# Performance work log

Hardware: AMD Instinct MI355X
Metric: run time of the kernel (lower is better)

The kernel has to match this reference:

```python
import jax, jax.numpy as jnp
import numpy as np

STRIDES = (8, 16, 32)
BINS = 16
NC = 80
ALPHA, GAMMA = 0.25, 2.0
W_CLS, W_IOU, W_DFL = 1.0, 7.5, 1.5
B, MAX_GT = 32, 32
EPS = 1e-7


def setup_inputs() -> dict:
    key = jax.random.key(0)
    k0, k1, k2, k3, k4, k5, k6 = jax.random.split(key, 7)
    p0 = jax.random.normal(k0, (B, 4 * BINS + NC, 80, 80), dtype=jnp.float32)
    p1 = jax.random.normal(k1, (B, 4 * BINS + NC, 40, 40), dtype=jnp.float32)
    p2 = jax.random.normal(k2, (B, 4 * BINS + NC, 20, 20), dtype=jnp.float32)
    # realistic xyxy boxes inside a 640x640 image
    c = jax.random.uniform(k3, (B, MAX_GT, 2), minval=60.0, maxval=580.0)
    wh = jax.random.uniform(k4, (B, MAX_GT, 2), minval=16.0, maxval=120.0)
    gt_bboxes = jnp.concatenate([c - wh / 2, c + wh / 2], axis=-1).astype(jnp.float32)
    gt_labels = jax.random.randint(k5, (B, MAX_GT), 0, NC, dtype=jnp.int32)
    raw = jax.random.randint(k6, (B, 8400), 0, 20 * MAX_GT, dtype=jnp.int32)
    matched_gt_inds = jnp.where(raw < MAX_GT, raw, -1)
    return {"p0": p0, "p1": p1, "p2": p2, "gt_bboxes": gt_bboxes,
            "gt_labels": gt_labels, "matched_gt_inds": matched_gt_inds}


def _decode_scale(p, stride):
    # p: [B, 4*BINS + NC, H, W]
    Bp, C, H, W = p.shape
    dfl = p[:, :4 * BINS].reshape(Bp, 4, BINS, H, W)
    cls = p[:, 4 * BINS:]
    # DFL decode: expectation of softmax over bins, scaled by stride
    prob = jax.nn.softmax(dfl, axis=2)
    proj = jnp.arange(BINS, dtype=p.dtype)
    dist = jnp.einsum('bkchw,c->bkhw', prob, proj) * stride  # [B,4,H,W] in pixels
    ys, xs = jnp.meshgrid(jnp.arange(H), jnp.arange(W), indexing='ij')
    cx = ((xs.astype(p.dtype)) + 0.5) * stride
    cy = ((ys.astype(p.dtype)) + 0.5) * stride
    boxes = jnp.stack([cx - dist[:, 0], cy - dist[:, 1],
                       cx + dist[:, 2], cy + dist[:, 3]], axis=-1).reshape(Bp, H * W, 4)
    cls_logits = cls.transpose(0, 2, 3, 1).reshape(Bp, H * W, NC)
    dfl_flat = dfl.transpose(0, 3, 4, 1, 2).reshape(Bp, H * W, 4, BINS)
    grid = jnp.stack([cx, cy], axis=-1).reshape(H * W, 2)
    smap = jnp.full((H * W,), stride, dtype=p.dtype)
    return cls_logits, dfl_flat, boxes, grid, smap


def reference(p0, p1, p2, gt_bboxes, gt_labels, matched_gt_inds):
    outs = [_decode_scale(p, s) for p, s in zip((p0, p1, p2), STRIDES)]
    scores = jnp.concatenate([o[0] for o in outs], axis=1)   # [B,N,NC]
    dfl = jnp.concatenate([o[1] for o in outs], axis=1)      # [B,N,4,BINS]
    pboxes = jnp.concatenate([o[2] for o in outs], axis=1)   # [B,N,4]
    grid = jnp.concatenate([o[3] for o in outs], axis=0)     # [N,2]
    smap = jnp.concatenate([o[4] for o in outs], axis=0)     # [N]

    pos = matched_gt_inds >= 0                               # [B,N]
    idx = jnp.where(pos, matched_gt_inds, 0)
    lbl = jnp.take_along_axis(gt_labels, idx, axis=1)        # [B,N]
    posf = pos.astype(scores.dtype)
    tgt_scores = jax.nn.one_hot(lbl, NC, dtype=scores.dtype) * posf[..., None]

    # sigmoid focal loss (stable BCE-with-logits)
    prob = jax.nn.sigmoid(scores)
    ce = jnp.maximum(scores, 0) - scores * tgt_scores + jnp.log1p(jnp.exp(-jnp.abs(scores)))
    p_t = prob * tgt_scores + (1 - prob) * (1 - tgt_scores)
    alpha_t = tgt_scores * ALPHA + (1 - tgt_scores) * (1 - ALPHA)
    cls_elem = alpha_t * (1.0 - p_t) ** GAMMA * ce
    num_pos = jnp.maximum(posf.sum(), 1.0)
    loss_cls = cls_elem.sum() / num_pos

    # gather matched GT boxes per anchor
    tboxes = jnp.take_along_axis(gt_bboxes, idx[..., None], axis=1)  # [B,N,4]
    gx, gy = grid[None, :, 0], grid[None, :, 1]
    l = jnp.clip(gx - tboxes[..., 0], 0.0)
    t = jnp.clip(gy - tboxes[..., 1], 0.0)
    r = jnp.clip(tboxes[..., 2] - gx, 0.0)
    b_ = jnp.clip(tboxes[..., 3] - gy, 0.0)
    dists = jnp.stack([l, t, r, b_], axis=-1) / smap[None, :, None]   # [B,N,4]
    tb = jnp.clip(dists, 0.0, BINS - 1 - 1e-6)
    lo = jnp.floor(tb).astype(jnp.int32)
    hi = jnp.minimum(lo + 1, BINS - 1)
    a = tb - lo.astype(tb.dtype)
    # soft two-bin DFL target (vectorized form of the scatter_add loop)
    tdist = (jax.nn.one_hot(lo, BINS, dtype=dfl.dtype) * (1.0 - a)[..., None]
             + jax.nn.one_hot(hi, BINS, dtype=dfl.dtype) * a[..., None])   # [B,N,4,BINS]
    logp = jax.nn.log_softmax(dfl, axis=-1)
    dfl_elem = -(tdist * logp).sum(-1)                                # [B,N,4]
    loss_dfl = (dfl_elem * posf[..., None]).sum() / (num_pos * 4.0)

    # IoU loss on positives
    ix1 = jnp.maximum(pboxes[..., 0], tboxes[..., 0])
    iy1 = jnp.maximum(pboxes[..., 1], tboxes[..., 1])
    ix2 = jnp.minimum(pboxes[..., 2], tboxes[..., 2])
    iy2 = jnp.minimum(pboxes[..., 3], tboxes[..., 3])
    inter = jnp.clip(ix2 - ix1, 0.0) * jnp.clip(iy2 - iy1, 0.0)
    area_p = jnp.clip(pboxes[..., 2] - pboxes[..., 0], 0.0) * jnp.clip(pboxes[..., 3] - pboxes[..., 1], 0.0)
    area_t = jnp.clip(tboxes[..., 2] - tboxes[..., 0], 0.0) * jnp.clip(tboxes[..., 3] - tboxes[..., 1], 0.0)
    iou = inter / (area_p + area_t - inter + EPS)
    loss_iou = ((1.0 - iou) * posf).sum() / num_pos

    total = W_CLS * loss_cls + W_IOU * loss_iou + W_DFL * loss_dfl
    return total
```

## Files before the change

kernel.cpp:

```cpp
#include <hip/hip_runtime.h>
#include <math.h>

#define NCLS 80
#define BINS 16
#define BATCH 32
#define MAX_GT 32
#define NA 8400
#define AN (BATCH * NA)
#define NT 2100
#define NB_DFL 1050
#define NB_CLS 2560
#define NSLOT 64
#define ALPHA_C 0.25f
#define W_CLS 1.0
#define W_IOU 7.5
#define W_DFL 1.5
#define EPS_F 1e-7f


__device__ __forceinline__ void block_reduce_atomic(float val, double* __restrict__ target)
{
    __shared__ float s[4];
    __syncthreads();
    #pragma unroll
    for (int o = 32; o > 0; o >>= 1) val += __shfl_down(val, o);
    const int wave = threadIdx.x >> 6, lane = threadIdx.x & 63;
    if (lane == 0) s[wave] = val;
    __syncthreads();
    if (threadIdx.x == 0) atomicAdd(target, (double)(s[0] + s[1] + s[2] + s[3]));
}

__device__ __forceinline__ float focal_elem(float s, float tt)
{
    float e   = __expf(-fabsf(s));
    float inv = 1.f / (1.f + e);
    float prob = (s >= 0.f) ? inv : e * inv;
    float ce  = fmaxf(s, 0.f) - s * tt + __logf(1.f + e);
    float p_t = prob * tt + (1.f - prob) * (1.f - tt);
    float alpha_t = tt * ALPHA_C + (1.f - tt) * (1.f - ALPHA_C);
    float om = 1.f - p_t;
    return alpha_t * om * om * ce;
}

__global__ __launch_bounds__(256) void yolo_prep(
    const int* __restrict__ matched, const int* __restrict__ gt_labels,
    signed char* __restrict__ lblmap, double* __restrict__ acc)
{
    if (blockIdx.x == 0) acc[threadIdx.x] = 0.0;
    const int qid = blockIdx.x * 256 + threadIdx.x;
    if (qid >= AN / 4) return;
    const int a0 = qid * 4;
    const int b  = a0 / NA;
    const int4 m4 = *(const int4*)(matched + a0);
    const int mm[4] = {m4.x, m4.y, m4.z, m4.w};
    char4 o;
    o.x = (mm[0] >= 0) ? (signed char)gt_labels[b * MAX_GT + mm[0]] : (signed char)-1;
    o.y = (mm[1] >= 0) ? (signed char)gt_labels[b * MAX_GT + mm[1]] : (signed char)-1;
    o.z = (mm[2] >= 0) ? (signed char)gt_labels[b * MAX_GT + mm[2]] : (signed char)-1;
    o.w = (mm[3] >= 0) ? (signed char)gt_labels[b * MAX_GT + mm[3]] : (signed char)-1;
    *(char4*)(lblmap + a0) = o;
}

__global__ __launch_bounds__(256) void yolo_mega(
    const float* __restrict__ p0, const float* __restrict__ p1, const float* __restrict__ p2,
    const float* __restrict__ gt_bboxes, const int* __restrict__ matched,
    const signed char* __restrict__ lblmap, double* __restrict__ acc)
{
    const int bid  = blockIdx.x;
    const int slot = bid & (NSLOT - 1);

    if (bid < NB_DFL) {
        __shared__ float spd[64][4][4];
        const int gdt = bid * 256 + (int)threadIdx.x;
        const int k   = gdt & 3;
        const int qg  = gdt >> 2;
        const int b   = qg / NT;
        const int t   = qg - b * NT;

        const float* p; int HW, off, gbase, h, w0; float stride;
        if (t < 1600)      { p = p0; HW = 6400; off = t * 4;          gbase = 0;    stride = 8.f;
                             h = t / 20;  w0 = (t - h * 20) * 4; }
        else if (t < 2000) { p = p1; HW = 1600; off = (t - 1600) * 4; gbase = 6400; stride = 16.f;
                             int u = t - 1600; h = u / 10; w0 = (u - h * 10) * 4; }
        else               { p = p2; HW = 400;  off = (t - 2000) * 4; gbase = 8000; stride = 32.f;
                             int u = t - 2000; h = u / 5;  w0 = (u - h * 5) * 4; }
        const float inv_s = 1.f / stride;
        const float cy = ((float)h + 0.5f) * stride;

        const float* pc = p + (size_t)(b * 144 + k * BINS) * HW + off;
        float v[BINS][4];
        #pragma unroll
        for (int i = 0; i < BINS; ++i) {
            float4 q = *(const float4*)(pc + (size_t)i * HW);
            v[i][0] = q.x; v[i][1] = q.y; v[i][2] = q.z; v[i][3] = q.w;
        }
        const int4 m4 = *(const int4*)(matched + (size_t)b * NA + gbase + off);
        const int mm[4] = {m4.x, m4.y, m4.z, m4.w};
        bool pos[4]; float4 tbv[4]; float tdv[4];
        #pragma unroll
        for (int j = 0; j < 4; ++j) {
            pos[j] = (mm[j] >= 0);
            int idx = pos[j] ? mm[j] : 0;
            tbv[j] = *(const float4*)(gt_bboxes + ((size_t)b * MAX_GT + idx) * 4);
            float cx = ((float)(w0 + j) + 0.5f) * stride;
            float d = (k == 0) ? (cx - tbv[j].x) : (k == 1) ? (cy - tbv[j].y)
                    : (k == 2) ? (tbv[j].z - cx) : (tbv[j].w - cy);
            tdv[j] = fmaxf(d, 0.f) * inv_s;
        }

        float part = 0.f;
        float pd[4];
        #pragma unroll
        for (int j = 0; j < 4; ++j) {
            float tval = fminf(tdv[j], (float)(BINS - 1) - 1e-6f);
            int   lo = (int)floorf(tval);
            float fr = tval - (float)lo;
            float mx = v[0][j];
            #pragma unroll
            for (int i = 1; i < BINS; ++i) mx = fmaxf(mx, v[i][j]);
            float se = 0.f, we = 0.f, vlo = 0.f, vhi = 0.f;
            #pragma unroll
            for (int i = 0; i < BINS; ++i) {
                float e = __expf(v[i][j] - mx);
                se += e;
                we += (float)i * e;
                vlo = (i == lo)     ? v[i][j] : vlo;
                vhi = (i == lo + 1) ? v[i][j] : vhi;
            }
            pd[j] = (we / se) * stride;
            if (pos[j]) {
                float lse = mx + __logf(se);
                part += -((1.f - fr) * (vlo - lse) + fr * (vhi - lse));
            }
        }
        *(float4*)&spd[threadIdx.x >> 2][k][0] = make_float4(pd[0], pd[1], pd[2], pd[3]);
        __syncthreads();

        float iou_part = 0.f, cnt = 0.f;
        if (k == 0) {
            const int g = threadIdx.x >> 2;
            #pragma unroll
            for (int j = 0; j < 4; ++j) {
                if (pos[j]) {
                    float cx = ((float)(w0 + j) + 0.5f) * stride;
                    float px1 = cx - spd[g][0][j], py1 = cy - spd[g][1][j];
                    float px2 = cx + spd[g][2][j], py2 = cy + spd[g][3][j];
                    float4 tb = tbv[j];
                    float ix1 = fmaxf(px1, tb.x), iy1 = fmaxf(py1, tb.y);
                    float ix2 = fminf(px2, tb.z), iy2 = fminf(py2, tb.w);
                    float inter  = fmaxf(ix2 - ix1, 0.f) * fmaxf(iy2 - iy1, 0.f);
                    float area_p = fmaxf(px2 - px1, 0.f) * fmaxf(py2 - py1, 0.f);
                    float area_t = fmaxf(tb.z - tb.x, 0.f) * fmaxf(tb.w - tb.y, 0.f);
                    float iou = inter / (area_p + area_t - inter + EPS_F);
                    iou_part += 1.f - iou;
                    cnt += 1.f;
                }
            }
        }
        block_reduce_atomic(part,     &acc[2 * NSLOT + slot]);
        block_reduce_atomic(iou_part, &acc[1 * NSLOT + slot]);
        block_reduce_atomic(cnt,      &acc[3 * NSLOT + slot]);
    } else {
        const int cbid = bid - NB_DFL;
        const int b = cbid / NCLS;
        const int c = cbid - b * NCLS;
        const size_t cls_ch = (size_t)(b * 144 + 4 * BINS + c);
        const signed char* lb0 = lblmap + b * NA;

        float4 q[9];
        char4  l4[9];
        const float* pl0 = p0 + cls_ch * 6400;
        #pragma unroll
        for (int i = 0; i < 6; ++i) {
            int off = (i * 256 + (int)threadIdx.x) * 4;
            q[i]  = *(const float4*)(pl0 + off);
            l4[i] = *(const char4*)(lb0 + off);
        }
        #pragma unroll
        for (int i = 6; i < 9; ++i) {
            int t  = i * 256 + (int)threadIdx.x;
            int tc = (t < NT) ? t : 0;
            const float* p; int HW, off, gbase;
            if (tc < 1600)      { p = p0; HW = 6400; off = tc * 4;          gbase = 0;    }
            else if (tc < 2000) { p = p1; HW = 1600; off = (tc - 1600) * 4; gbase = 6400; }
            else                { p = p2; HW = 400;  off = (tc - 2000) * 4; gbase = 8000; }
            q[i]  = *(const float4*)(p + cls_ch * HW + off);
            l4[i] = *(const char4*)(lb0 + gbase + off);
        }

        float part = 0.f;
        #pragma unroll
        for (int i = 0; i < 9; ++i) {
            const bool valid = (i < 8) || (i * 256 + (int)threadIdx.x < NT);
            const float s4[4]  = {q[i].x, q[i].y, q[i].z, q[i].w};
            const int   lbl[4] = {l4[i].x, l4[i].y, l4[i].z, l4[i].w};
            float sum = 0.f;
            #pragma unroll
            for (int j = 0; j < 4; ++j)
                sum += focal_elem(s4[j], (c == lbl[j]) ? 1.f : 0.f);
            part += valid ? sum : 0.f;
        }
        block_reduce_atomic(part, &acc[0 * NSLOT + slot]);
    }
}

__global__ __launch_bounds__(256) void yolo_loss_fused(
    const float* __restrict__ p0, const float* __restrict__ p1, const float* __restrict__ p2,
    const float* __restrict__ gt_bboxes, const int* __restrict__ gt_labels,
    const int* __restrict__ matched, double* __restrict__ acc)
{
    const int a = blockIdx.x * blockDim.x + threadIdx.x;
    const int b = blockIdx.y;
    const int slot = blockIdx.x & (NSLOT - 1);
    float cls_acc = 0.f, iou_acc = 0.f, dfl_acc = 0.f, pos_cnt = 0.f;
    if (a < NA) {
        const float* p; int HW, W; float stride; int off;
        if (a < 6400)      { p = p0; HW = 6400; W = 80; stride = 8.f;  off = a; }
        else if (a < 8000) { p = p1; HW = 1600; W = 40; stride = 16.f; off = a - 6400; }
        else               { p = p2; HW = 400;  W = 20; stride = 32.f; off = a - 8000; }
        const int h = off / W, w = off - h * W;
        const float cx = ((float)w + 0.5f) * stride, cy = ((float)h + 0.5f) * stride;
        const float* pb = p + ((size_t)b * 144) * (size_t)HW + (size_t)off;
        const int m = matched[(size_t)b * NA + a];
        const bool pos = (m >= 0);
        const int idx = pos ? m : 0;
        const int lbl = gt_labels[b * MAX_GT + idx];
        const float* tbp = gt_bboxes + ((size_t)b * MAX_GT + idx) * 4;
        const float tx1 = tbp[0], ty1 = tbp[1], tx2 = tbp[2], ty2 = tbp[3];
        float tdist[4] = {fmaxf(cx - tx1, 0.f) / stride, fmaxf(cy - ty1, 0.f) / stride,
                          fmaxf(tx2 - cx, 0.f) / stride, fmaxf(ty2 - cy, 0.f) / stride};
        float pdv[4]; float dfl_sum = 0.f;
        #pragma unroll
        for (int k = 0; k < 4; ++k) {
            float tv = fminf(tdist[k], (float)(BINS - 1) - 1e-6f);
            int lo = (int)floorf(tv);
            float fr = tv - (float)lo;
            const float* pc = pb + (size_t)(k * BINS) * HW;
            float v[BINS];
            #pragma unroll
            for (int i = 0; i < BINS; ++i) v[i] = pc[(size_t)i * HW];
            float mx = v[0];
            #pragma unroll
            for (int i = 1; i < BINS; ++i) mx = fmaxf(mx, v[i]);
            float se = 0.f, we = 0.f, vlo = 0.f, vhi = 0.f;
            #pragma unroll
            for (int i = 0; i < BINS; ++i) {
                float e = __expf(v[i] - mx);
                se += e; we += (float)i * e;
                vlo = (i == lo) ? v[i] : vlo;
                vhi = (i == lo + 1) ? v[i] : vhi;
            }
            pdv[k] = (we / se) * stride;
            if (pos) { float lse = mx + __logf(se); dfl_sum += -((1.f - fr) * (vlo - lse) + fr * (vhi - lse)); }
        }
        const float* pcls = pb + (size_t)(4 * BINS) * HW;
        #pragma unroll 4
        for (int c = 0; c < NCLS; ++c)
            cls_acc += focal_elem(pcls[(size_t)c * HW], (pos && c == lbl) ? 1.f : 0.f);
        if (pos) {
            float px1 = cx - pdv[0], py1 = cy - pdv[1], px2 = cx + pdv[2], py2 = cy + pdv[3];
            float ix1 = fmaxf(px1, tx1), iy1 = fmaxf(py1, ty1);
            float ix2 = fminf(px2, tx2), iy2 = fminf(py2, ty2);
            float inter  = fmaxf(ix2 - ix1, 0.f) * fmaxf(iy2 - iy1, 0.f);
            float area_p = fmaxf(px2 - px1, 0.f) * fmaxf(py2 - py1, 0.f);
            float area_t = fmaxf(tx2 - tx1, 0.f) * fmaxf(ty2 - ty1, 0.f);
            float iou = inter / (area_p + area_t - inter + EPS_F);
            iou_acc = 1.f - iou; dfl_acc = dfl_sum; pos_cnt = 1.f;
        }
    }
    block_reduce_atomic(cls_acc, &acc[0 * NSLOT + slot]);
    block_reduce_atomic(iou_acc, &acc[1 * NSLOT + slot]);
    block_reduce_atomic(dfl_acc, &acc[2 * NSLOT + slot]);
    block_reduce_atomic(pos_cnt, &acc[3 * NSLOT + slot]);
}

__global__ void yolo_loss_finalize(const double* __restrict__ acc, float* __restrict__ out)
{
    double s[4] = {0.0, 0.0, 0.0, 0.0};
    for (int q = 0; q < 4; ++q)
        for (int i = 0; i < NSLOT; ++i) s[q] += acc[q * NSLOT + i];
    double np = s[3] < 1.0 ? 1.0 : s[3];
    double total = W_CLS * s[0] / np + W_IOU * s[1] / np + W_DFL * s[2] / (np * 4.0);
    out[0] = (float)total;
}

extern "C" void kernel_launch(void* const* d_in, const int* in_sizes, int n_in,
                              void* d_out, int out_size, void* d_ws, size_t ws_size,
                              hipStream_t stream)
{
    const float* p0        = (const float*)d_in[0];
    const float* p1        = (const float*)d_in[1];
    const float* p2        = (const float*)d_in[2];
    const float* gt_bboxes = (const float*)d_in[3];
    const int*   gt_labels = (const int*)d_in[4];
    const int*   matched   = (const int*)d_in[5];
    float*  out = (float*)d_out;

    const size_t accBytes = 4 * NSLOT * sizeof(double);
    double*      acc    = (double*)d_ws;
    signed char* lblmap = (signed char*)((char*)d_ws + accBytes);
    const size_t need = accBytes + (size_t)AN;

    if (ws_size >= need) {
        yolo_prep<<<(AN / 4 + 255) / 256, 256, 0, stream>>>(matched, gt_labels, lblmap, acc);
        yolo_mega<<<NB_DFL + NB_CLS, 256, 0, stream>>>(p0, p1, p2, gt_bboxes, matched,
                                                       lblmap, acc);
    } else {
        (void)hipMemsetAsync(acc, 0, accBytes, stream);
        dim3 g((NA + 255) / 256, BATCH);
        yolo_loss_fused<<<g, 256, 0, stream>>>(p0, p1, p2, gt_bboxes, gt_labels, matched, acc);
    }
    yolo_loss_finalize<<<1, 1, 0, stream>>>(acc, out);
}
```

Measured before the change: 213.5 us.

## Use 1024-thread blocks with online softmax for DFL and split class planes

Blocks of the fused loss kernel grow from 256 to 1024 threads. In the DFL branch, each of the four side groups now covers 256 quads. The 16-bin softmax becomes an online, streaming max/sum instead of holding all 64 values in registers, which cuts register pressure so more waves fit. The class branch splits each plane into two halves handled by a strided loop rather than fully unrolled preloads. Block reductions now sum 16 wave partials. The trade-offs are extra exp work from the online rescaling, lower memory-level parallelism per thread, and a second gt_bboxes load for the IoU step.

```diff
diff --git a/kernel.cpp b/kernel.cpp
--- a/kernel.cpp
+++ b/kernel.cpp
@@ -8,8 +8,9 @@
 #define NA 8400
 #define AN (BATCH * NA)
 #define NT 2100
-#define NB_DFL 1050
-#define NB_CLS 2560
+#define NQG (BATCH * NT)
+#define NB_DFL 263
+#define NB_CLS 5120
 #define NSLOT 64
 #define ALPHA_C 0.25f
 #define W_CLS 1.0
@@ -18,7 +19,24 @@
 #define EPS_F 1e-7f
 
 
-__device__ __forceinline__ void block_reduce_atomic(float val, double* __restrict__ target)
+__device__ __forceinline__ void block_reduce_atomic_16(float val, double* __restrict__ target)
+{
+    __shared__ float s[16];
+    __syncthreads();
+    #pragma unroll
+    for (int o = 32; o > 0; o >>= 1) val += __shfl_down(val, o);
+    const int wave = threadIdx.x >> 6, lane = threadIdx.x & 63;
+    if (lane == 0) s[wave] = val;
+    __syncthreads();
+    if (threadIdx.x == 0) {
+        float t = 0.f;
+        #pragma unroll
+        for (int i = 0; i < 16; ++i) t += s[i];
+        atomicAdd(target, (double)t);
+    }
+}
+
+__device__ __forceinline__ void block_reduce_atomic_4(float val, double* __restrict__ target)
 {
     __shared__ float s[4];
     __syncthreads();
@@ -40,6 +58,17 @@
     float alpha_t = tt * ALPHA_C + (1.f - tt) * (1.f - ALPHA_C);
     float om = 1.f - p_t;
     return alpha_t * om * om * ce;
+}
+
+__device__ __forceinline__ void quad_map(int t, int& HW, int& off, int& gbase,
+                                         int& h, int& w0, float& stride)
+{
+    if (t < 1600)      { HW = 6400; off = t * 4;          gbase = 0;    stride = 8.f;
+                         h = t / 20;  w0 = (t - h * 20) * 4; }
+    else if (t < 2000) { HW = 1600; off = (t - 1600) * 4; gbase = 6400; stride = 16.f;
+                         int u = t - 1600; h = u / 10; w0 = (u - h * 10) * 4; }
+    else               { HW = 400;  off = (t - 2000) * 4; gbase = 8000; stride = 32.f;
+                         int u = t - 2000; h = u / 5;  w0 = (u - h * 5) * 4; }
 }
 
 __global__ __launch_bounds__(256) void yolo_prep(
@@ -61,7 +90,7 @@
     *(char4*)(lblmap + a0) = o;
 }
 
-__global__ __launch_bounds__(256) void yolo_mega(
+__global__ __launch_bounds__(1024, 8) void yolo_mega(
     const float* __restrict__ p0, const float* __restrict__ p1, const float* __restrict__ p2,
     const float* __restrict__ gt_bboxes, const int* __restrict__ matched,
     const signed char* __restrict__ lblmap, double* __restrict__ acc)
@@ -70,82 +99,89 @@
     const int slot = bid & (NSLOT - 1);
 
     if (bid < NB_DFL) {
-        __shared__ float spd[64][4][4];
-        const int gdt = bid * 256 + (int)threadIdx.x;
-        const int k   = gdt & 3;
-        const int qg  = gdt >> 2;
-        const int b   = qg / NT;
-        const int t   = qg - b * NT;
-
-        const float* p; int HW, off, gbase, h, w0; float stride;
-        if (t < 1600)      { p = p0; HW = 6400; off = t * 4;          gbase = 0;    stride = 8.f;
-                             h = t / 20;  w0 = (t - h * 20) * 4; }
-        else if (t < 2000) { p = p1; HW = 1600; off = (t - 1600) * 4; gbase = 6400; stride = 16.f;
-                             int u = t - 1600; h = u / 10; w0 = (u - h * 10) * 4; }
-        else               { p = p2; HW = 400;  off = (t - 2000) * 4; gbase = 8000; stride = 32.f;
-                             int u = t - 2000; h = u / 5;  w0 = (u - h * 5) * 4; }
+        __shared__ float4 spd[4][256];
+        const int local = threadIdx.x & 255;
+        const int k     = threadIdx.x >> 8;
+        const int qg    = bid * 256 + local;
+        const bool valid = (qg < NQG);
+        const int qv = valid ? qg : 0;
+        const int b  = qv / NT;
+        const int t  = qv - b * NT;
+
+        int HW, off, gbase, h, w0; float stride;
+        quad_map(t, HW, off, gbase, h, w0, stride);
         const float inv_s = 1.f / stride;
         const float cy = ((float)h + 0.5f) * stride;
-
-        const float* pc = p + (size_t)(b * 144 + k * BINS) * HW + off;
-        float v[BINS][4];
-        #pragma unroll
-        for (int i = 0; i < BINS; ++i) {
-            float4 q = *(const float4*)(pc + (size_t)i * HW);
-            v[i][0] = q.x; v[i][1] = q.y; v[i][2] = q.z; v[i][3] = q.w;
-        }
+        const float* p = (t < 1600) ? p0 : (t < 2000) ? p1 : p2;
+
         const int4 m4 = *(const int4*)(matched + (size_t)b * NA + gbase + off);
         const int mm[4] = {m4.x, m4.y, m4.z, m4.w};
-        bool pos[4]; float4 tbv[4]; float tdv[4];
+        int lo[4]; float fr[4]; bool pos[4];
         #pragma unroll
         for (int j = 0; j < 4; ++j) {
             pos[j] = (mm[j] >= 0);
             int idx = pos[j] ? mm[j] : 0;
-            tbv[j] = *(const float4*)(gt_bboxes + ((size_t)b * MAX_GT + idx) * 4);
+            float4 tb = *(const float4*)(gt_bboxes + ((size_t)b * MAX_GT + idx) * 4);
             float cx = ((float)(w0 + j) + 0.5f) * stride;
-            float d = (k == 0) ? (cx - tbv[j].x) : (k == 1) ? (cy - tbv[j].y)
-                    : (k == 2) ? (tbv[j].z - cx) : (tbv[j].w - cy);
-            tdv[j] = fmaxf(d, 0.f) * inv_s;
+            float d = (k == 0) ? (cx - tb.x) : (k == 1) ? (cy - tb.y)
+                    : (k == 2) ? (tb.z - cx) : (tb.w - cy);
+            float tval = fminf(fmaxf(d, 0.f) * inv_s, (float)(BINS - 1) - 1e-6f);
+            lo[j] = (int)floorf(tval);
+            fr[j] = tval - (float)lo[j];
+        }
+
+        const float* pc = p + (size_t)(b * 144 + k * BINS) * HW + off;
+        float mx[4], se[4], we[4], vlo[4], vhi[4];
+        #pragma unroll
+        for (int j = 0; j < 4; ++j) { mx[j] = -1e30f; se[j] = 0.f; we[j] = 0.f; vlo[j] = 0.f; vhi[j] = 0.f; }
+
+        #pragma unroll 4
+        for (int i = 0; i < BINS; ++i) {
+            float4 q = {0.f, 0.f, 0.f, 0.f};
+            if (valid) q = *(const float4*)(pc + (size_t)i * HW);
+            const float vj[4] = {q.x, q.y, q.z, q.w};
+            #pragma unroll
+            for (int j = 0; j < 4; ++j) {
+                float v = vj[j];
+                float nm = fmaxf(mx[j], v);
+                float scale = __expf(mx[j] - nm);
+                float e = __expf(v - nm);
+                se[j] = se[j] * scale + e;
+                we[j] = we[j] * scale + (float)i * e;
+                mx[j] = nm;
+                vlo[j] = (i == lo[j])     ? v : vlo[j];
+                vhi[j] = (i == lo[j] + 1) ? v : vhi[j];
+            }
         }
 
         float part = 0.f;
         float pd[4];
         #pragma unroll
         for (int j = 0; j < 4; ++j) {
-            float tval = fminf(tdv[j], (float)(BINS - 1) - 1e-6f);
-            int   lo = (int)floorf(tval);
-            float fr = tval - (float)lo;
-            float mx = v[0][j];
-            #pragma unroll
-            for (int i = 1; i < BINS; ++i) mx = fmaxf(mx, v[i][j]);
-            float se = 0.f, we = 0.f, vlo = 0.f, vhi = 0.f;
-            #pragma unroll
-            for (int i = 0; i < BINS; ++i) {
-                float e = __expf(v[i][j] - mx);
-                se += e;
-                we += (float)i * e;
-                vlo = (i == lo)     ? v[i][j] : vlo;
-                vhi = (i == lo + 1) ? v[i][j] : vhi;
+            pd[j] = (we[j] / se[j]) * stride;
+            if (valid && pos[j]) {
+                float lse = mx[j] + __logf(se[j]);
+                part += -((1.f - fr[j]) * (vlo[j] - lse) + fr[j] * (vhi[j] - lse));
             }
-            pd[j] = (we / se) * stride;
-            if (pos[j]) {
-                float lse = mx + __logf(se);
-                part += -((1.f - fr) * (vlo - lse) + fr * (vhi - lse));
-            }
-        }
-        *(float4*)&spd[threadIdx.x >> 2][k][0] = make_float4(pd[0], pd[1], pd[2], pd[3]);
+        }
+        spd[k][local] = make_float4(pd[0], pd[1], pd[2], pd[3]);
         __syncthreads();
 
         float iou_part = 0.f, cnt = 0.f;
-        if (k == 0) {
-            const int g = threadIdx.x >> 2;
+        if (k == 0 && valid) {
+            const float4 q0 = spd[0][local], q1 = spd[1][local];
+            const float4 q2 = spd[2][local], q3 = spd[3][local];
+            const float l_[4] = {q0.x, q0.y, q0.z, q0.w};
+            const float t_[4] = {q1.x, q1.y, q1.z, q1.w};
+            const float r_[4] = {q2.x, q2.y, q2.z, q2.w};
+            const float b_[4] = {q3.x, q3.y, q3.z, q3.w};
             #pragma unroll
             for (int j = 0; j < 4; ++j) {
                 if (pos[j]) {
+                    float4 tb = *(const float4*)(gt_bboxes + ((size_t)b * MAX_GT + mm[j]) * 4);
                     float cx = ((float)(w0 + j) + 0.5f) * stride;
-                    float px1 = cx - spd[g][0][j], py1 = cy - spd[g][1][j];
-                    float px2 = cx + spd[g][2][j], py2 = cy + spd[g][3][j];
-                    float4 tb = tbv[j];
+                    float px1 = cx - l_[j], py1 = cy - t_[j];
+                    float px2 = cx + r_[j], py2 = cy + b_[j];
                     float ix1 = fmaxf(px1, tb.x), iy1 = fmaxf(py1, tb.y);
                     float ix2 = fminf(px2, tb.z), iy2 = fminf(py2, tb.w);
                     float inter  = fmaxf(ix2 - ix1, 0.f) * fmaxf(iy2 - iy1, 0.f);
@@ -157,50 +193,34 @@
                 }
             }
         }
-        block_reduce_atomic(part,     &acc[2 * NSLOT + slot]);
-        block_reduce_atomic(iou_part, &acc[1 * NSLOT + slot]);
-        block_reduce_atomic(cnt,      &acc[3 * NSLOT + slot]);
+        block_reduce_atomic_16(part,     &acc[2 * NSLOT + slot]);
+        block_reduce_atomic_16(iou_part, &acc[1 * NSLOT + slot]);
+        block_reduce_atomic_16(cnt,      &acc[3 * NSLOT + slot]);
     } else {
-        const int cbid = bid - NB_DFL;
-        const int b = cbid / NCLS;
-        const int c = cbid - b * NCLS;
+        const int cbid  = bid - NB_DFL;
+        const int half  = cbid & 1;
+        const int plane = cbid >> 1;
+        const int b = plane / NCLS;
+        const int c = plane - b * NCLS;
         const size_t cls_ch = (size_t)(b * 144 + 4 * BINS + c);
         const signed char* lb0 = lblmap + b * NA;
 
-        float4 q[9];
-        char4  l4[9];
-        const float* pl0 = p0 + cls_ch * 6400;
-        #pragma unroll
-        for (int i = 0; i < 6; ++i) {
-            int off = (i * 256 + (int)threadIdx.x) * 4;
-            q[i]  = *(const float4*)(pl0 + off);
-            l4[i] = *(const char4*)(lb0 + off);
-        }
-        #pragma unroll
-        for (int i = 6; i < 9; ++i) {
-            int t  = i * 256 + (int)threadIdx.x;
-            int tc = (t < NT) ? t : 0;
+        float part = 0.f;
+        for (int q = (int)threadIdx.x; q < 1050; q += 1024) {
+            const int t = half * 1050 + q;
             const float* p; int HW, off, gbase;
-            if (tc < 1600)      { p = p0; HW = 6400; off = tc * 4;          gbase = 0;    }
-            else if (tc < 2000) { p = p1; HW = 1600; off = (tc - 1600) * 4; gbase = 6400; }
-            else                { p = p2; HW = 400;  off = (tc - 2000) * 4; gbase = 8000; }
-            q[i]  = *(const float4*)(p + cls_ch * HW + off);
-            l4[i] = *(const char4*)(lb0 + gbase + off);
-        }
-
-        float part = 0.f;
-        #pragma unroll
-        for (int i = 0; i < 9; ++i) {
-            const bool valid = (i < 8) || (i * 256 + (int)threadIdx.x < NT);
-            const float s4[4]  = {q[i].x, q[i].y, q[i].z, q[i].w};
-            const int   lbl[4] = {l4[i].x, l4[i].y, l4[i].z, l4[i].w};
-            float sum = 0.f;
-            #pragma unroll
-            for (int j = 0; j < 4; ++j)
-                sum += focal_elem(s4[j], (c == lbl[j]) ? 1.f : 0.f);
-            part += valid ? sum : 0.f;
-        }
-        block_reduce_atomic(part, &acc[0 * NSLOT + slot]);
+            if (t < 1600)      { p = p0; HW = 6400; off = t * 4;          gbase = 0;    }
+            else if (t < 2000) { p = p1; HW = 1600; off = (t - 1600) * 4; gbase = 6400; }
+            else               { p = p2; HW = 400;  off = (t - 2000) * 4; gbase = 8000; }
+
+            float4 s4 = *(const float4*)(p + cls_ch * HW + off);
+            char4  l4 = *(const char4*)(lb0 + gbase + off);
+            part += focal_elem(s4.x, (c == l4.x) ? 1.f : 0.f);
+            part += focal_elem(s4.y, (c == l4.y) ? 1.f : 0.f);
+            part += focal_elem(s4.z, (c == l4.z) ? 1.f : 0.f);
+            part += focal_elem(s4.w, (c == l4.w) ? 1.f : 0.f);
+        }
+        block_reduce_atomic_16(part, &acc[0 * NSLOT + slot]);
     }
 }
 
@@ -268,10 +288,10 @@
             iou_acc = 1.f - iou; dfl_acc = dfl_sum; pos_cnt = 1.f;
         }
     }
-    block_reduce_atomic(cls_acc, &acc[0 * NSLOT + slot]);
-    block_reduce_atomic(iou_acc, &acc[1 * NSLOT + slot]);
-    block_reduce_atomic(dfl_acc, &acc[2 * NSLOT + slot]);
-    block_reduce_atomic(pos_cnt, &acc[3 * NSLOT + slot]);
+    block_reduce_atomic_4(cls_acc, &acc[0 * NSLOT + slot]);
+    block_reduce_atomic_4(iou_acc, &acc[1 * NSLOT + slot]);
+    block_reduce_atomic_4(dfl_acc, &acc[2 * NSLOT + slot]);
+    block_reduce_atomic_4(pos_cnt, &acc[3 * NSLOT + slot]);
 }
 
 __global__ void yolo_loss_finalize(const double* __restrict__ acc, float* __restrict__ out)
@@ -303,8 +323,8 @@
 
     if (ws_size >= need) {
         yolo_prep<<<(AN / 4 + 255) / 256, 256, 0, stream>>>(matched, gt_labels, lblmap, acc);
-        yolo_mega<<<NB_DFL + NB_CLS, 256, 0, stream>>>(p0, p1, p2, gt_bboxes, matched,
-                                                       lblmap, acc);
+        yolo_mega<<<NB_DFL + NB_CLS, 1024, 0, stream>>>(p0, p1, p2, gt_bboxes, matched,
+                                                        lblmap, acc);
     } else {
         (void)hipMemsetAsync(acc, 0, accBytes, stream);
         dim3 g((NA + 255) / 256, BATCH);
```

Result: slower. 228.2 us (+6.9%).
